# Performance work log

Measured on AMD Instinct MI355X. Metric: run time of the kernel, lower is better.

## Reference

```python
import jax, jax.numpy as jnp
import numpy as np

NUM_ASPECTS = 5
CTX_WIN = 3
H1 = 10
WORD_DIM = 300
REVIEW_LEN = 500
BATCH = 512


def setup_inputs() -> dict:
    key = jax.random.key(0)
    k1, k2, k3 = jax.random.split(key, 3)
    review_emb = jax.random.normal(k1, (BATCH, REVIEW_LEN, WORD_DIM), dtype=jnp.float32)
    # learned params (original inits uniform(-0.01, 0.01))
    asp_embed = jax.random.uniform(k2, (NUM_ASPECTS, CTX_WIN * H1), dtype=jnp.float32,
                                   minval=-0.01, maxval=0.01)
    asp_proj = jax.random.uniform(k3, (NUM_ASPECTS, WORD_DIM, H1), dtype=jnp.float32,
                                  minval=-0.01, maxval=0.01)
    return {"review_emb": review_emb, "asp_embed": asp_embed, "asp_proj": asp_proj}


def reference(review_emb, asp_embed, asp_proj):
    # review_emb: (b, l, d); asp_proj: (a, d, h); asp_embed: (a, ctx*h)
    A, D, H = asp_proj.shape
    ctx = asp_embed.shape[1] // H
    pad = (ctx - 1) // 2
    L = review_emb.shape[1]

    # per-aspect projection: (b, a, l, h)
    proj = jnp.einsum('bld,adh->balh', review_emb, asp_proj)

    # windowed context score: score[b,a,l] = sum_{w,h} proj_padded[b,a,l+w,h] * E[a,w,h]
    # (equals torch unfold(ctx)->view(ctx*h) matmul with aspEmbed, since unfold+transpose
    #  yields [ctx, h] flattened order)
    padded = jnp.pad(proj, ((0, 0), (0, 0), (pad, pad), (0, 0)))
    E = asp_embed.reshape(A, ctx, H)
    score = sum(jnp.einsum('balh,ah->bal', padded[:, :, w:w + L, :], E[:, w, :])
                for w in range(ctx))  # small fixed ctx loop; avoids materializing unfold

    # softmax over review length (torch: dim=1 of (b*?, L, 1))
    attn = jax.nn.softmax(score, axis=2)  # (b, a, l)

    # weighted pooling
    rep = jnp.einsum('bal,balh->bah', attn, proj)  # (b, a, h)
    return attn, rep
```

## Files before the change

### kernel.cpp

```cpp
#include <hip/hip_runtime.h>

#define B_   512
#define L_   500
#define D_   300
#define A_   5
#define H_   10

__device__ __forceinline__ unsigned f2bf(float f) {
    union { float f; unsigned u; } c; c.f = f;
    unsigned r = c.u;
    r += 0x7fffu + ((r >> 16) & 1u);
    return r >> 16;
}
__device__ __forceinline__ float bf2f(unsigned u16) {
    union { unsigned u; float f; } c; c.u = u16 << 16;
    return c.f;
}

__global__ __launch_bounds__(320) void k_proj(const float* __restrict__ X,
                                              const float* __restrict__ W,
                                              unsigned short* __restrict__ P)
{
    __shared__ float lx[256][30];
    __shared__ float lwt[30][50];

    const int b    = blockIdx.y;
    const int l0   = blockIdx.x << 8;
    const int tid  = threadIdx.x;
    const int av   = tid >> 6;
    const int lane = tid & 63;
    const int kk_s = tid & 31;
    const int rg   = tid >> 5;

    float acc[4][10];
#pragma unroll
    for (int i = 0; i < 4; ++i)
#pragma unroll
        for (int j = 0; j < 10; ++j) acc[i][j] = 0.f;

    for (int c = 0; c < 10; ++c) {
        const int k0 = c * 30;

        if (kk_s < 30) {
            for (int r = rg; r < 256; r += 10) {
                const int gl = l0 + r;
                float v = 0.f;
                if (gl < L_) v = X[(b * L_ + gl) * D_ + k0 + kk_s];
                lx[r][kk_s] = v;
            }
        }
        for (int i = tid; i < 1500; i += 320) {
            const int kk = i / 50;
            const int hh = i - kk * 50;
            const int a2 = hh / 10;
            const int h2 = hh - a2 * 10;
            lwt[kk][hh] = W[(a2 * D_ + k0 + kk) * H_ + h2];
        }
        __syncthreads();

#pragma unroll 3
        for (int kk = 0; kk < 30; kk += 2) {
            float2 wlo[5], whi[5];
#pragma unroll
            for (int j = 0; j < 5; ++j) {
                wlo[j] = *(const float2*)&lwt[kk    ][av * 10 + 2 * j];
                whi[j] = *(const float2*)&lwt[kk + 1][av * 10 + 2 * j];
            }
#pragma unroll
            for (int ri = 0; ri < 4; ++ri) {
                const float2 x2 = *(const float2*)&lx[(ri << 6) + lane][kk];
#pragma unroll
                for (int j = 0; j < 5; ++j) {
                    acc[ri][2*j]   = fmaf(x2.x, wlo[j].x, acc[ri][2*j]);
                    acc[ri][2*j]   = fmaf(x2.y, whi[j].x, acc[ri][2*j]);
                    acc[ri][2*j+1] = fmaf(x2.x, wlo[j].y, acc[ri][2*j+1]);
                    acc[ri][2*j+1] = fmaf(x2.y, whi[j].y, acc[ri][2*j+1]);
                }
            }
        }
        __syncthreads();
    }

#pragma unroll
    for (int ri = 0; ri < 4; ++ri) {
        const int gl = l0 + (ri << 6) + lane;
        if (gl < L_) {
            unsigned* dst = (unsigned*)(P + ((size_t)((b * A_ + av) * L_ + gl)) * H_);
#pragma unroll
            for (int j = 0; j < 5; ++j) {
                const unsigned lo = f2bf(acc[ri][2*j]);
                const unsigned hi = f2bf(acc[ri][2*j+1]);
                dst[j] = lo | (hi << 16);
            }
        }
    }
}

__global__ __launch_bounds__(256) void k_attn(const unsigned short* __restrict__ P,
                                              const float* __restrict__ E,
                                              float* __restrict__ out)
{
    __shared__ float lp[L_][H_];
    __shared__ float red_m[4];
    __shared__ float red_z[4];
    __shared__ float red10[4][10];

    const int a    = blockIdx.x;
    const int b    = blockIdx.y;
    const int t    = threadIdx.x;
    const int wid  = t >> 6;
    const int lane = t & 63;

    const uint4* src = (const uint4*)(P + ((size_t)(b * A_ + a)) * L_ * H_);
    float* lpf = (float*)lp;
    for (int i = t; i < 625; i += 256) {
        const uint4 v = src[i];
        const int o = i * 8;
        lpf[o + 0] = bf2f(v.x & 0xffffu); lpf[o + 1] = bf2f(v.x >> 16);
        lpf[o + 2] = bf2f(v.y & 0xffffu); lpf[o + 3] = bf2f(v.y >> 16);
        lpf[o + 4] = bf2f(v.z & 0xffffu); lpf[o + 5] = bf2f(v.z >> 16);
        lpf[o + 6] = bf2f(v.w & 0xffffu); lpf[o + 7] = bf2f(v.w >> 16);
    }

    float e[3][10];
#pragma unroll
    for (int w = 0; w < 3; ++w)
#pragma unroll
        for (int h = 0; h < 10; ++h)
            e[w][h] = E[a * 30 + w * 10 + h];

    __syncthreads();

    const int l1 = t + 256;
    float s0 = 0.f, s1 = 0.f;
#pragma unroll
    for (int w = 0; w < 3; ++w) {
        const int lw0 = t + w - 1;
        if (lw0 >= 0 && lw0 < L_) {
#pragma unroll
            for (int h = 0; h < 10; ++h) s0 = fmaf(lp[lw0][h], e[w][h], s0);
        }
        const int lw1 = l1 + w - 1;
        if (l1 < L_ && lw1 < L_) {
#pragma unroll
            for (int h = 0; h < 10; ++h) s1 = fmaf(lp[lw1][h], e[w][h], s1);
        }
    }
    const bool has1 = (l1 < L_);

    float m = has1 ? fmaxf(s0, s1) : s0;
#pragma unroll
    for (int off = 32; off >= 1; off >>= 1) m = fmaxf(m, __shfl_xor(m, off));
    if (lane == 0) red_m[wid] = m;
    __syncthreads();
    m = fmaxf(fmaxf(red_m[0], red_m[1]), fmaxf(red_m[2], red_m[3]));

    const float e0 = expf(s0 - m);
    const float e1 = has1 ? expf(s1 - m) : 0.f;
    float z = e0 + e1;
#pragma unroll
    for (int off = 32; off >= 1; off >>= 1) z += __shfl_xor(z, off);
    if (lane == 0) red_z[wid] = z;
    __syncthreads();
    const float Z   = red_z[0] + red_z[1] + red_z[2] + red_z[3];
    const float inv = 1.f / Z;

    float* attn_out = out + (size_t)(b * A_ + a) * L_;
    const float a0 = e0 * inv;
    attn_out[t] = a0;
    float a1 = 0.f;
    if (has1) { a1 = e1 * inv; attn_out[l1] = a1; }

    float ph[10];
#pragma unroll
    for (int h = 0; h < 10; ++h) {
        float v = a0 * lp[t][h];
        if (has1) v = fmaf(a1, lp[l1][h], v);
        ph[h] = v;
    }
#pragma unroll
    for (int h = 0; h < 10; ++h) {
#pragma unroll
        for (int off = 32; off >= 1; off >>= 1) ph[h] += __shfl_xor(ph[h], off);
    }
    if (lane == 0) {
#pragma unroll
        for (int h = 0; h < 10; ++h) red10[wid][h] = ph[h];
    }
    __syncthreads();
    if (t < 10) {
        const float r = red10[0][t] + red10[1][t] + red10[2][t] + red10[3][t];
        out[(size_t)B_ * A_ * L_ + (size_t)(b * A_ + a) * H_ + t] = r;
    }
}

extern "C" void kernel_launch(void* const* d_in, const int* in_sizes, int n_in,
                              void* d_out, int out_size, void* d_ws, size_t ws_size,
                              hipStream_t stream)
{
    const float* X = (const float*)d_in[0];
    const float* E = (const float*)d_in[1];
    const float* W = (const float*)d_in[2];
    float* out = (float*)d_out;
    unsigned short* P = (unsigned short*)d_ws;

    dim3 g1(2, B_), b1(320);
    k_proj<<<g1, b1, 0, stream>>>(X, W, P);

    dim3 g2(A_, B_), b2(256);
    k_attn<<<g2, b2, 0, stream>>>(P, E, out);
}
```

Baseline: 731.3 us.

## Fuse projection and attention softmax pooling into one per-batch kernel

Replaces the two-kernel pipeline (projection writing bf16 P to global workspace, then attention per (batch, aspect)) with a single kernel per batch row. Each thread owns one review position, streams its 300-dim row of X directly from global with float4 loads and a software prefetch, and multiplies by the full 300x50 weight held in LDS. The bf16 projections stay in shared memory for the windowed score, softmax and pooling. This removes the workspace round trip and the second launch. In exchange it uses a large LDS footprint (about 116 KB) and 50 accumulators per thread, which lowers occupancy, and each thread's X loads are strided 1200 bytes apart across lanes, so they do not coalesce.

```diff
diff --git a/kernel.cpp b/kernel.cpp
--- a/kernel.cpp
+++ b/kernel.cpp
@@ -5,6 +5,9 @@
 #define D_   300
 #define A_   5
 #define H_   10
+#define NJ   50
+#define WROW 52
+#define PROW 27
 
 __device__ __forceinline__ unsigned f2bf(float f) {
     union { float f; unsigned u; } c; c.f = f;
@@ -17,180 +20,173 @@
     return c.f;
 }
 
-__global__ __launch_bounds__(320) void k_proj(const float* __restrict__ X,
-                                              const float* __restrict__ W,
-                                              unsigned short* __restrict__ P)
+__device__ __forceinline__ float wred_max(float v) {
+#pragma unroll
+    for (int off = 32; off >= 1; off >>= 1) v = fmaxf(v, __shfl_xor(v, off));
+    return v;
+}
+__device__ __forceinline__ float wred_sum(float v) {
+#pragma unroll
+    for (int off = 32; off >= 1; off >>= 1) v += __shfl_xor(v, off);
+    return v;
+}
+
+__global__ __launch_bounds__(512) void k_fused(const float* __restrict__ X,
+                                               const float* __restrict__ E,
+                                               const float* __restrict__ W,
+                                               float* __restrict__ out)
 {
-    __shared__ float lx[256][30];
-    __shared__ float lwt[30][50];
-
-    const int b    = blockIdx.y;
-    const int l0   = blockIdx.x << 8;
-    const int tid  = threadIdx.x;
-    const int av   = tid >> 6;
-    const int lane = tid & 63;
-    const int kk_s = tid & 31;
-    const int rg   = tid >> 5;
-
-    float acc[4][10];
-#pragma unroll
-    for (int i = 0; i < 4; ++i)
-#pragma unroll
-        for (int j = 0; j < 10; ++j) acc[i][j] = 0.f;
-
-    for (int c = 0; c < 10; ++c) {
-        const int k0 = c * 30;
-
-        if (kk_s < 30) {
-            for (int r = rg; r < 256; r += 10) {
-                const int gl = l0 + r;
-                float v = 0.f;
-                if (gl < L_) v = X[(b * L_ + gl) * D_ + k0 + kk_s];
-                lx[r][kk_s] = v;
-            }
-        }
-        for (int i = tid; i < 1500; i += 320) {
-            const int kk = i / 50;
-            const int hh = i - kk * 50;
-            const int a2 = hh / 10;
-            const int h2 = hh - a2 * 10;
-            lwt[kk][hh] = W[(a2 * D_ + k0 + kk) * H_ + h2];
-        }
-        __syncthreads();
-
-#pragma unroll 3
-        for (int kk = 0; kk < 30; kk += 2) {
-            float2 wlo[5], whi[5];
-#pragma unroll
-            for (int j = 0; j < 5; ++j) {
-                wlo[j] = *(const float2*)&lwt[kk    ][av * 10 + 2 * j];
-                whi[j] = *(const float2*)&lwt[kk + 1][av * 10 + 2 * j];
-            }
-#pragma unroll
-            for (int ri = 0; ri < 4; ++ri) {
-                const float2 x2 = *(const float2*)&lx[(ri << 6) + lane][kk];
-#pragma unroll
-                for (int j = 0; j < 5; ++j) {
-                    acc[ri][2*j]   = fmaf(x2.x, wlo[j].x, acc[ri][2*j]);
-                    acc[ri][2*j]   = fmaf(x2.y, whi[j].x, acc[ri][2*j]);
-                    acc[ri][2*j+1] = fmaf(x2.x, wlo[j].y, acc[ri][2*j+1]);
-                    acc[ri][2*j+1] = fmaf(x2.y, whi[j].y, acc[ri][2*j+1]);
-                }
-            }
-        }
-        __syncthreads();
-    }
-
-#pragma unroll
-    for (int ri = 0; ri < 4; ++ri) {
-        const int gl = l0 + (ri << 6) + lane;
-        if (gl < L_) {
-            unsigned* dst = (unsigned*)(P + ((size_t)((b * A_ + av) * L_ + gl)) * H_);
-#pragma unroll
-            for (int j = 0; j < 5; ++j) {
-                const unsigned lo = f2bf(acc[ri][2*j]);
-                const unsigned hi = f2bf(acc[ri][2*j+1]);
-                dst[j] = lo | (hi << 16);
-            }
-        }
-    }
-}
-
-__global__ __launch_bounds__(256) void k_attn(const unsigned short* __restrict__ P,
-                                              const float* __restrict__ E,
-                                              float* __restrict__ out)
-{
-    __shared__ float lp[L_][H_];
-    __shared__ float red_m[4];
-    __shared__ float red_z[4];
-    __shared__ float red10[4][10];
-
-    const int a    = blockIdx.x;
-    const int b    = blockIdx.y;
+    __shared__ __align__(16) float ws_w[D_ * WROW];
+    __shared__ unsigned ws_p[L_ * PROW];
+    __shared__ float ws_e[160];
+    __shared__ float redbuf[8][NJ];
+
+    const int b    = blockIdx.x;
     const int t    = threadIdx.x;
     const int wid  = t >> 6;
     const int lane = t & 63;
-
-    const uint4* src = (const uint4*)(P + ((size_t)(b * A_ + a)) * L_ * H_);
-    float* lpf = (float*)lp;
-    for (int i = t; i < 625; i += 256) {
-        const uint4 v = src[i];
-        const int o = i * 8;
-        lpf[o + 0] = bf2f(v.x & 0xffffu); lpf[o + 1] = bf2f(v.x >> 16);
-        lpf[o + 2] = bf2f(v.y & 0xffffu); lpf[o + 3] = bf2f(v.y >> 16);
-        lpf[o + 4] = bf2f(v.z & 0xffffu); lpf[o + 5] = bf2f(v.z >> 16);
-        lpf[o + 6] = bf2f(v.w & 0xffffu); lpf[o + 7] = bf2f(v.w >> 16);
-    }
-
-    float e[3][10];
-#pragma unroll
-    for (int w = 0; w < 3; ++w)
-#pragma unroll
-        for (int h = 0; h < 10; ++h)
-            e[w][h] = E[a * 30 + w * 10 + h];
-
-    __syncthreads();
-
-    const int l1 = t + 256;
-    float s0 = 0.f, s1 = 0.f;
-#pragma unroll
-    for (int w = 0; w < 3; ++w) {
-        const int lw0 = t + w - 1;
-        if (lw0 >= 0 && lw0 < L_) {
-#pragma unroll
-            for (int h = 0; h < 10; ++h) s0 = fmaf(lp[lw0][h], e[w][h], s0);
-        }
-        const int lw1 = l1 + w - 1;
-        if (l1 < L_ && lw1 < L_) {
-#pragma unroll
-            for (int h = 0; h < 10; ++h) s1 = fmaf(lp[lw1][h], e[w][h], s1);
-        }
-    }
-    const bool has1 = (l1 < L_);
-
-    float m = has1 ? fmaxf(s0, s1) : s0;
-#pragma unroll
-    for (int off = 32; off >= 1; off >>= 1) m = fmaxf(m, __shfl_xor(m, off));
-    if (lane == 0) red_m[wid] = m;
-    __syncthreads();
-    m = fmaxf(fmaxf(red_m[0], red_m[1]), fmaxf(red_m[2], red_m[3]));
-
-    const float e0 = expf(s0 - m);
-    const float e1 = has1 ? expf(s1 - m) : 0.f;
-    float z = e0 + e1;
-#pragma unroll
-    for (int off = 32; off >= 1; off >>= 1) z += __shfl_xor(z, off);
-    if (lane == 0) red_z[wid] = z;
-    __syncthreads();
-    const float Z   = red_z[0] + red_z[1] + red_z[2] + red_z[3];
-    const float inv = 1.f / Z;
-
-    float* attn_out = out + (size_t)(b * A_ + a) * L_;
-    const float a0 = e0 * inv;
-    attn_out[t] = a0;
-    float a1 = 0.f;
-    if (has1) { a1 = e1 * inv; attn_out[l1] = a1; }
-
-    float ph[10];
-#pragma unroll
-    for (int h = 0; h < 10; ++h) {
-        float v = a0 * lp[t][h];
-        if (has1) v = fmaf(a1, lp[l1][h], v);
-        ph[h] = v;
-    }
-#pragma unroll
-    for (int h = 0; h < 10; ++h) {
-#pragma unroll
-        for (int off = 32; off >= 1; off >>= 1) ph[h] += __shfl_xor(ph[h], off);
-    }
-    if (lane == 0) {
-#pragma unroll
-        for (int h = 0; h < 10; ++h) red10[wid][h] = ph[h];
-    }
-    __syncthreads();
-    if (t < 10) {
-        const float r = red10[0][t] + red10[1][t] + red10[2][t] + red10[3][t];
-        out[(size_t)B_ * A_ * L_ + (size_t)(b * A_ + a) * H_ + t] = r;
+    const bool valid = (t < L_);
+
+    const float4* xrow = (const float4*)(X + (size_t)(b * L_ + (valid ? t : 0)) * D_);
+    float4 xb0 = xrow[0], xb1 = xrow[1], xb2 = xrow[2];
+
+    for (int i = t; i < D_ * NJ; i += 512) {
+        const int k = i / NJ, r = i - k * NJ;
+        const int a = r / H_, h = r - a * H_;
+        ws_w[k * WROW + r] = W[(a * D_ + k) * H_ + h];
+    }
+    if (t < A_ * 30) ws_e[t] = E[t];
+    __syncthreads();
+
+    if (valid) {
+        float acc[NJ];
+#pragma unroll
+        for (int j = 0; j < NJ; ++j) acc[j] = 0.f;
+
+#pragma unroll 1
+        for (int it = 0; it < 25; ++it) {
+            const int nb = (it < 24) ? (it + 1) * 3 : 72;
+            const float4 xn0 = xrow[nb], xn1 = xrow[nb + 1], xn2 = xrow[nb + 2];
+            const int k0 = it * 12;
+#pragma unroll
+            for (int q = 0; q < 3; ++q) {
+                const float4 xq = (q == 0) ? xb0 : ((q == 1) ? xb1 : xb2);
+#pragma unroll
+                for (int c = 0; c < 4; ++c) {
+                    const float xs = (c == 0) ? xq.x : ((c == 1) ? xq.y : ((c == 2) ? xq.z : xq.w));
+                    const float* wr = &ws_w[(k0 + q * 4 + c) * WROW];
+#pragma unroll
+                    for (int j4 = 0; j4 < 12; ++j4) {
+                        const float4 wv = *(const float4*)&wr[j4 * 4];
+                        acc[j4*4+0] = fmaf(xs, wv.x, acc[j4*4+0]);
+                        acc[j4*4+1] = fmaf(xs, wv.y, acc[j4*4+1]);
+                        acc[j4*4+2] = fmaf(xs, wv.z, acc[j4*4+2]);
+                        acc[j4*4+3] = fmaf(xs, wv.w, acc[j4*4+3]);
+                    }
+                    const float2 wt = *(const float2*)&wr[48];
+                    acc[48] = fmaf(xs, wt.x, acc[48]);
+                    acc[49] = fmaf(xs, wt.y, acc[49]);
+                }
+            }
+            xb0 = xn0; xb1 = xn1; xb2 = xn2;
+        }
+
+#pragma unroll
+        for (int u = 0; u < 25; ++u) {
+            const unsigned lo = f2bf(acc[2*u]), hi = f2bf(acc[2*u+1]);
+            ws_p[t * PROW + u] = lo | (hi << 16);
+        }
+    }
+    __syncthreads();
+
+    float sc[A_];
+    if (valid) {
+#pragma unroll
+        for (int a = 0; a < A_; ++a) {
+            float s = 0.f;
+#pragma unroll
+            for (int w = 0; w < 3; ++w) {
+                const int lw = t + w - 1;
+                if (lw >= 0 && lw < L_) {
+#pragma unroll
+                    for (int u = 0; u < 5; ++u) {
+                        const unsigned pv = ws_p[lw * PROW + a * 5 + u];
+                        s = fmaf(bf2f(pv & 0xffffu), ws_e[a*30 + w*10 + 2*u],     s);
+                        s = fmaf(bf2f(pv >> 16),     ws_e[a*30 + w*10 + 2*u + 1], s);
+                    }
+                }
+            }
+            sc[a] = s;
+        }
+    } else {
+#pragma unroll
+        for (int a = 0; a < A_; ++a) sc[a] = -1e30f;
+    }
+
+#pragma unroll
+    for (int a = 0; a < A_; ++a) {
+        const float m = wred_max(sc[a]);
+        if (lane == 0) redbuf[wid][a] = m;
+    }
+    __syncthreads();
+    float mB[A_];
+#pragma unroll
+    for (int a = 0; a < A_; ++a) {
+        float m = redbuf[0][a];
+#pragma unroll
+        for (int w2 = 1; w2 < 8; ++w2) m = fmaxf(m, redbuf[w2][a]);
+        mB[a] = m;
+    }
+    __syncthreads();
+
+    float eB[A_];
+#pragma unroll
+    for (int a = 0; a < A_; ++a) {
+        eB[a] = valid ? __expf(sc[a] - mB[a]) : 0.f;
+        const float z = wred_sum(eB[a]);
+        if (lane == 0) redbuf[wid][a] = z;
+    }
+    __syncthreads();
+
+    float att[A_];
+    float* aout = out + (size_t)b * (A_ * L_);
+#pragma unroll
+    for (int a = 0; a < A_; ++a) {
+        float Z = 0.f;
+#pragma unroll
+        for (int w2 = 0; w2 < 8; ++w2) Z += redbuf[w2][a];
+        att[a] = eB[a] * (1.0f / Z);
+        if (valid) aout[a * L_ + t] = att[a];
+    }
+    __syncthreads();
+
+    float p50[NJ];
+    if (valid) {
+#pragma unroll
+        for (int a = 0; a < A_; ++a) {
+            const float aa = att[a];
+#pragma unroll
+            for (int u = 0; u < 5; ++u) {
+                const unsigned pv = ws_p[t * PROW + a * 5 + u];
+                p50[a*10 + 2*u]     = aa * bf2f(pv & 0xffffu);
+                p50[a*10 + 2*u + 1] = aa * bf2f(pv >> 16);
+            }
+        }
+    } else {
+#pragma unroll
+        for (int j = 0; j < NJ; ++j) p50[j] = 0.f;
+    }
+#pragma unroll
+    for (int j = 0; j < NJ; ++j) {
+        const float r = wred_sum(p50[j]);
+        if (lane == 0) redbuf[wid][j] = r;
+    }
+    __syncthreads();
+    if (t < NJ) {
+        float r = 0.f;
+#pragma unroll
+        for (int w2 = 0; w2 < 8; ++w2) r += redbuf[w2][t];
+        out[(size_t)B_ * A_ * L_ + (size_t)b * NJ + t] = r;
     }
 }
 
@@ -202,11 +198,6 @@
     const float* E = (const float*)d_in[1];
     const float* W = (const float*)d_in[2];
     float* out = (float*)d_out;
-    unsigned short* P = (unsigned short*)d_ws;
-
-    dim3 g1(2, B_), b1(320);
-    k_proj<<<g1, b1, 0, stream>>>(X, W, P);
-
-    dim3 g2(A_, B_), b2(256);
-    k_attn<<<g2, b2, 0, stream>>>(P, E, out);
-}
+
+    k_fused<<<B_, 512, 0, stream>>>(X, E, W, out);
+}
```

Result: faster. 699.5 us (-4.4%).
